# Optimization experiments

Measured on AMD Instinct MI355X. Metric: run time of the kernel, lower is better.

Reference implementation:

```python
import jax, jax.numpy as jnp
import numpy as np

N, D, R = 65536, 32, 128


def setup_inputs() -> dict:
    key = jax.random.key(0)
    k1, k2, k3, k4 = jax.random.split(key, 4)
    X = jax.random.normal(k1, (N, D), dtype=jnp.float32)
    a = jax.random.normal(k2, (R, D), dtype=jnp.float32)
    b = jax.random.uniform(k3, (R, D), dtype=jnp.float32)  # positive, like abs(randn)
    c = jax.random.normal(k4, (R, D + 1), dtype=jnp.float32)
    return {"X": X, "a": a, "b": b, "c": c}


def reference(X, a, b, c):
    # Gaussian membership per (sample, rule, dim): exp(-(x-a)^2 / (2*clamp(b,1e-8)^2))
    b_cl = jnp.clip(b, 1e-8)                      # [R, D]
    diff = X[:, None, :] - a[None, :, :]          # [N, R, D]
    mu = jnp.exp(-(diff * diff) / (2.0 * b_cl * b_cl))
    strengths = jnp.prod(mu, axis=2)              # [N, R] rule firing strengths
    strengths_sum = jnp.sum(strengths, axis=1, keepdims=True)
    normalized = strengths / (strengths_sum + 1e-8)
    # consequent: linear model per rule, X @ c[:, :-1].T + bias
    rule_out = X @ c[:, :-1].T + c[:, -1]         # [N, R]
    predictions = jnp.sum(normalized * rule_out, axis=1)  # [N]
    return (predictions, strengths, normalized)
```

## Files before the change

kernel.cpp:

```cpp
#include <hip/hip_runtime.h>

#define NS 65536
#define DD 32
#define RR 128
#define SPB 16
#define STR 132

__global__ __launch_bounds__(128, 4) void anfis_main(
    const float* __restrict__ X, const float* __restrict__ A,
    const float* __restrict__ B, const float* __restrict__ C,
    float* __restrict__ out_pred, float* __restrict__ out_str,
    float* __restrict__ out_norm)
{
    __shared__ float SBUF[SPB * STR];
    __shared__ float PBUF[SPB * STR];
    __shared__ float pS[SPB][8];
    __shared__ float pD[SPB][8];
    __shared__ float scale_lds[SPB];

    const int tid   = threadIdx.x;
    const int nbase = blockIdx.x * SPB;

    float w_[DD], naw_[DD], ck_[DD], bias;
    {
        const float4* av = (const float4*)(A + tid * DD);
        const float4* bv = (const float4*)(B + tid * DD);
        #pragma unroll
        for (int i = 0; i < 8; ++i) {
            float4 va = av[i], vb = bv[i];
            float w0 = 0.8493218003f * __builtin_amdgcn_rcpf(fmaxf(vb.x, 1e-8f));
            float w1 = 0.8493218003f * __builtin_amdgcn_rcpf(fmaxf(vb.y, 1e-8f));
            float w2 = 0.8493218003f * __builtin_amdgcn_rcpf(fmaxf(vb.z, 1e-8f));
            float w3 = 0.8493218003f * __builtin_amdgcn_rcpf(fmaxf(vb.w, 1e-8f));
            w_[4*i+0] = w0; naw_[4*i+0] = -va.x * w0;
            w_[4*i+1] = w1; naw_[4*i+1] = -va.y * w1;
            w_[4*i+2] = w2; naw_[4*i+2] = -va.z * w2;
            w_[4*i+3] = w3; naw_[4*i+3] = -va.w * w3;
        }
        #pragma unroll
        for (int d = 0; d < DD; ++d) ck_[d] = C[tid * (DD + 1) + d];
        bias = C[tid * (DD + 1) + DD];
    }
    #pragma unroll
    for (int d = 0; d < DD; ++d)
        asm("" : "+v"(w_[d]), "+v"(naw_[d]), "+v"(ck_[d]));
    asm("" : "+v"(bias));

    const float* Xg = X + (size_t)nbase * DD;

    float xa[DD], xb[DD];
#define LOADX(arr, jj) { _Pragma("unroll") \
    for (int i = 0; i < DD; ++i) arr[i] = Xg[(jj) * DD + i]; }

#define COMPUTE(arr, jj) { \
    float s0 = 0.f, s1 = 0.f, s2 = 0.f, s3 = 0.f; \
    float r0 = bias, r1 = 0.f, r2 = 0.f, r3 = 0.f; \
    _Pragma("unroll") \
    for (int d = 0; d < DD; d += 4) { \
        float t0 = fmaf(arr[d+0], w_[d+0], naw_[d+0]); s0 = fmaf(t0, t0, s0); r0 = fmaf(arr[d+0], ck_[d+0], r0); \
        float t1 = fmaf(arr[d+1], w_[d+1], naw_[d+1]); s1 = fmaf(t1, t1, s1); r1 = fmaf(arr[d+1], ck_[d+1], r1); \
        float t2 = fmaf(arr[d+2], w_[d+2], naw_[d+2]); s2 = fmaf(t2, t2, s2); r2 = fmaf(arr[d+2], ck_[d+2], r2); \
        float t3 = fmaf(arr[d+3], w_[d+3], naw_[d+3]); s3 = fmaf(t3, t3, s3); r3 = fmaf(arr[d+3], ck_[d+3], r3); \
    } \
    float st = __builtin_amdgcn_exp2f(-((s0 + s1) + (s2 + s3))); \
    float ro = (r0 + r1) + (r2 + r3); \
    SBUF[(jj) * STR + tid] = st; \
    PBUF[(jj) * STR + tid] = st * ro; }

    LOADX(xa, 0)
    for (int j = 0; j < SPB; j += 2) {
        LOADX(xb, j + 1)
        COMPUTE(xa, j)
        if (j + 2 < SPB) LOADX(xa, j + 2)
        COMPUTE(xb, j + 1)
    }
#undef LOADX
#undef COMPUTE
    __syncthreads();

    {
        int s = tid >> 3, o = tid & 7;
        const float4* srow = (const float4*)&SBUF[s * STR + o * 16];
        const float4* prow = (const float4*)&PBUF[s * STR + o * 16];
        float ss = 0.f, dd = 0.f;
        #pragma unroll
        for (int k = 0; k < 4; ++k) {
            float4 v = srow[k]; ss += (v.x + v.y) + (v.z + v.w);
            float4 p = prow[k]; dd += (p.x + p.y) + (p.z + p.w);
        }
        pS[s][o] = ss; pD[s][o] = dd;
    }
    __syncthreads();
    if (tid < SPB) {
        float ss = 0.f, dd = 0.f;
        #pragma unroll
        for (int o = 0; o < 8; ++o) { ss += pS[tid][o]; dd += pD[tid][o]; }
        float sc = 1.0f / (ss + 1e-8f);
        out_pred[nbase + tid] = dd * sc;
        scale_lds[tid] = sc;
    }
    __syncthreads();

    #pragma unroll
    for (int it = 0; it < 4; ++it) {
        int f   = it * 128 + tid;
        int row = f >> 5;
        int col = f & 31;
        float4 v = *(const float4*)&SBUF[row * STR + col * 4];
        float sc = scale_lds[row];
        size_t base = ((size_t)(nbase + row)) * RR + col * 4;
        *(float4*)(out_str  + base) = v;
        *(float4*)(out_norm + base) = make_float4(v.x * sc, v.y * sc, v.z * sc, v.w * sc);
    }
}

extern "C" void kernel_launch(void* const* d_in, const int* in_sizes, int n_in,
                              void* d_out, int out_size, void* d_ws, size_t ws_size,
                              hipStream_t stream) {
    const float* X = (const float*)d_in[0];
    const float* A = (const float*)d_in[1];
    const float* B = (const float*)d_in[2];
    const float* C = (const float*)d_in[3];

    float* pred = (float*)d_out;
    float* str  = pred + NS;
    float* nrm  = str + (size_t)NS * RR;

    anfis_main<<<dim3(NS / SPB), dim3(128), 0, stream>>>(X, A, B, C, pred, str, nrm);
}
```

Baseline: 107.0 us.

## Split membership and consequent passes to cut register pressure, vector X loads

```diff
diff --git a/kernel.cpp b/kernel.cpp
--- a/kernel.cpp
+++ b/kernel.cpp
@@ -5,6 +5,7 @@
 #define RR 128
 #define SPB 16
 #define STR 132
+#define NQ (SPB * 4)
 
 __global__ __launch_bounds__(128, 4) void anfis_main(
     const float* __restrict__ X, const float* __restrict__ A,
@@ -21,61 +22,104 @@
     const int tid   = threadIdx.x;
     const int nbase = blockIdx.x * SPB;
 
-    float w_[DD], naw_[DD], ck_[DD], bias;
+    int vzero = 0;
+    asm("" : "+v"(vzero));
+    const float* xp = X + (size_t)nbase * DD + vzero;
+
     {
-        const float4* av = (const float4*)(A + tid * DD);
-        const float4* bv = (const float4*)(B + tid * DD);
+        float w_[DD], naw_[DD];
+        {
+            const float4* av = (const float4*)(A + tid * DD);
+            const float4* bv = (const float4*)(B + tid * DD);
+            #pragma unroll
+            for (int i = 0; i < 8; ++i) {
+                float4 va = av[i], vb = bv[i];
+                float w0 = 0.8493218003f * __builtin_amdgcn_rcpf(fmaxf(vb.x, 1e-8f));
+                float w1 = 0.8493218003f * __builtin_amdgcn_rcpf(fmaxf(vb.y, 1e-8f));
+                float w2 = 0.8493218003f * __builtin_amdgcn_rcpf(fmaxf(vb.z, 1e-8f));
+                float w3 = 0.8493218003f * __builtin_amdgcn_rcpf(fmaxf(vb.w, 1e-8f));
+                w_[4*i+0] = w0; naw_[4*i+0] = -va.x * w0;
+                w_[4*i+1] = w1; naw_[4*i+1] = -va.y * w1;
+                w_[4*i+2] = w2; naw_[4*i+2] = -va.z * w2;
+                w_[4*i+3] = w3; naw_[4*i+3] = -va.w * w3;
+            }
+        }
         #pragma unroll
-        for (int i = 0; i < 8; ++i) {
-            float4 va = av[i], vb = bv[i];
-            float w0 = 0.8493218003f * __builtin_amdgcn_rcpf(fmaxf(vb.x, 1e-8f));
-            float w1 = 0.8493218003f * __builtin_amdgcn_rcpf(fmaxf(vb.y, 1e-8f));
-            float w2 = 0.8493218003f * __builtin_amdgcn_rcpf(fmaxf(vb.z, 1e-8f));
-            float w3 = 0.8493218003f * __builtin_amdgcn_rcpf(fmaxf(vb.w, 1e-8f));
-            w_[4*i+0] = w0; naw_[4*i+0] = -va.x * w0;
-            w_[4*i+1] = w1; naw_[4*i+1] = -va.y * w1;
-            w_[4*i+2] = w2; naw_[4*i+2] = -va.z * w2;
-            w_[4*i+3] = w3; naw_[4*i+3] = -va.w * w3;
+        for (int d = 0; d < DD; ++d) asm("" : "+v"(w_[d]), "+v"(naw_[d]));
+
+        float4 q[4][2];
+        #pragma unroll
+        for (int k = 0; k < 3; ++k) {
+            const float4* p = (const float4*)(xp + k * 8);
+            q[k][0] = p[0]; q[k][1] = p[1];
         }
+        float s0 = 0.f, s1 = 0.f, s2 = 0.f, s3 = 0.f;
+        #pragma unroll
+        for (int k = 0; k < NQ; ++k) {
+            if (k + 3 < NQ) {
+                const float4* p = (const float4*)(xp + (k + 3) * 8);
+                q[(k + 3) & 3][0] = p[0]; q[(k + 3) & 3][1] = p[1];
+            }
+            const int d0 = (k & 3) * 8;
+            float4 v0 = q[k & 3][0], v1 = q[k & 3][1];
+            float t0 = fmaf(v0.x, w_[d0+0], naw_[d0+0]); s0 = fmaf(t0, t0, s0);
+            float t1 = fmaf(v0.y, w_[d0+1], naw_[d0+1]); s1 = fmaf(t1, t1, s1);
+            float t2 = fmaf(v0.z, w_[d0+2], naw_[d0+2]); s2 = fmaf(t2, t2, s2);
+            float t3 = fmaf(v0.w, w_[d0+3], naw_[d0+3]); s3 = fmaf(t3, t3, s3);
+            float t4 = fmaf(v1.x, w_[d0+4], naw_[d0+4]); s0 = fmaf(t4, t4, s0);
+            float t5 = fmaf(v1.y, w_[d0+5], naw_[d0+5]); s1 = fmaf(t5, t5, s1);
+            float t6 = fmaf(v1.z, w_[d0+6], naw_[d0+6]); s2 = fmaf(t6, t6, s2);
+            float t7 = fmaf(v1.w, w_[d0+7], naw_[d0+7]); s3 = fmaf(t7, t7, s3);
+            if ((k & 3) == 3) {
+                float st = __builtin_amdgcn_exp2f(-((s0 + s1) + (s2 + s3)));
+                SBUF[(k >> 2) * STR + tid] = st;
+                s0 = s1 = s2 = s3 = 0.f;
+            }
+        }
+    }
+
+    __builtin_amdgcn_sched_barrier(0);
+
+    {
+        float ck_[DD], bias;
         #pragma unroll
         for (int d = 0; d < DD; ++d) ck_[d] = C[tid * (DD + 1) + d];
         bias = C[tid * (DD + 1) + DD];
+        #pragma unroll
+        for (int d = 0; d < DD; ++d) asm("" : "+v"(ck_[d]));
+        asm("" : "+v"(bias));
+
+        float4 q[4][2];
+        #pragma unroll
+        for (int k = 0; k < 3; ++k) {
+            const float4* p = (const float4*)(xp + k * 8);
+            q[k][0] = p[0]; q[k][1] = p[1];
+        }
+        float r0 = bias, r1 = 0.f, r2 = 0.f, r3 = 0.f;
+        #pragma unroll
+        for (int k = 0; k < NQ; ++k) {
+            if (k + 3 < NQ) {
+                const float4* p = (const float4*)(xp + (k + 3) * 8);
+                q[(k + 3) & 3][0] = p[0]; q[(k + 3) & 3][1] = p[1];
+            }
+            const int d0 = (k & 3) * 8;
+            float4 v0 = q[k & 3][0], v1 = q[k & 3][1];
+            r0 = fmaf(v0.x, ck_[d0+0], r0);
+            r1 = fmaf(v0.y, ck_[d0+1], r1);
+            r2 = fmaf(v0.z, ck_[d0+2], r2);
+            r3 = fmaf(v0.w, ck_[d0+3], r3);
+            r0 = fmaf(v1.x, ck_[d0+4], r0);
+            r1 = fmaf(v1.y, ck_[d0+5], r1);
+            r2 = fmaf(v1.z, ck_[d0+6], r2);
+            r3 = fmaf(v1.w, ck_[d0+7], r3);
+            if ((k & 3) == 3) {
+                const int j = k >> 2;
+                float st = SBUF[j * STR + tid];
+                PBUF[j * STR + tid] = st * ((r0 + r1) + (r2 + r3));
+                r0 = bias; r1 = r2 = r3 = 0.f;
+            }
+        }
     }
-    #pragma unroll
-    for (int d = 0; d < DD; ++d)
-        asm("" : "+v"(w_[d]), "+v"(naw_[d]), "+v"(ck_[d]));
-    asm("" : "+v"(bias));
-
-    const float* Xg = X + (size_t)nbase * DD;
-
-    float xa[DD], xb[DD];
-#define LOADX(arr, jj) { _Pragma("unroll") \
-    for (int i = 0; i < DD; ++i) arr[i] = Xg[(jj) * DD + i]; }
-
-#define COMPUTE(arr, jj) { \
-    float s0 = 0.f, s1 = 0.f, s2 = 0.f, s3 = 0.f; \
-    float r0 = bias, r1 = 0.f, r2 = 0.f, r3 = 0.f; \
-    _Pragma("unroll") \
-    for (int d = 0; d < DD; d += 4) { \
-        float t0 = fmaf(arr[d+0], w_[d+0], naw_[d+0]); s0 = fmaf(t0, t0, s0); r0 = fmaf(arr[d+0], ck_[d+0], r0); \
-        float t1 = fmaf(arr[d+1], w_[d+1], naw_[d+1]); s1 = fmaf(t1, t1, s1); r1 = fmaf(arr[d+1], ck_[d+1], r1); \
-        float t2 = fmaf(arr[d+2], w_[d+2], naw_[d+2]); s2 = fmaf(t2, t2, s2); r2 = fmaf(arr[d+2], ck_[d+2], r2); \
-        float t3 = fmaf(arr[d+3], w_[d+3], naw_[d+3]); s3 = fmaf(t3, t3, s3); r3 = fmaf(arr[d+3], ck_[d+3], r3); \
-    } \
-    float st = __builtin_amdgcn_exp2f(-((s0 + s1) + (s2 + s3))); \
-    float ro = (r0 + r1) + (r2 + r3); \
-    SBUF[(jj) * STR + tid] = st; \
-    PBUF[(jj) * STR + tid] = st * ro; }
-
-    LOADX(xa, 0)
-    for (int j = 0; j < SPB; j += 2) {
-        LOADX(xb, j + 1)
-        COMPUTE(xa, j)
-        if (j + 2 < SPB) LOADX(xa, j + 2)
-        COMPUTE(xb, j + 1)
-    }
-#undef LOADX
-#undef COMPUTE
     __syncthreads();
 
     {
```

Measured after the change: 160.9 us. +50.4%, slower.
